# Kernel optimization log

Hardware: AMD Instinct MI355X
Metric: run time of the kernel (lower is better)

## Reference

```python
import jax, jax.numpy as jnp
import numpy as np

WS = 32          # window_size
STRIDE = 16
OUTPUT = 224
GRADE_N = 6

def _dct_mat(size):
    i = np.arange(size)[:, None]
    j = np.arange(size)[None, :]
    scale = np.where(i == 0, np.sqrt(1.0 / size), np.sqrt(2.0 / size))
    return (scale * np.cos((j + 0.5) * np.pi * i / size)).astype(np.float32)

def _gen_filter(start, end, size):
    i = np.arange(size)[:, None]
    j = np.arange(size)[None, :]
    s = i + j
    return np.where((s > end) | (s < start), 0.0, 1.0).astype(np.float32)

# constant (non-learnable) buffers, derived from init hyperparams
_D = jnp.asarray(_dct_mat(WS))                       # [32,32]
_LEVEL_FILT = jnp.asarray(_gen_filter(0, WS * 2, WS))  # level_fliter=[0] -> band (0, 64)
_grade_filts = np.stack([_gen_filter(WS * 2.0 / GRADE_N * i, WS * 2.0 / GRADE_N * (i + 1), WS)
                         for i in range(GRADE_N)])    # [G,32,32]
_ft_num = _grade_filts.sum(axis=(1, 2))               # per-filter normalizer
_weights = (2.0 ** np.arange(GRADE_N)).astype(np.float32)  # w=1, *=2 each pass
_GRADE_FILT_SCALED = jnp.asarray(_grade_filts * (_weights / _ft_num)[:, None, None])  # [G,32,32]

def _unfold(x):
    # x: [B,C,H,W] -> patches [B,L,C,ws,ws], L row-major over (oh, ow), matching torch Unfold
    B, C, H, W = x.shape
    nH = (H - WS) // STRIDE + 1
    nW = (W - WS) // STRIDE + 1
    r = jnp.arange(nH) * STRIDE
    c = jnp.arange(nW) * STRIDE
    rows = r[:, None, None, None] + jnp.arange(WS)[None, None, :, None]  # [nH,1,ws,1]
    cols = c[None, :, None, None] + jnp.arange(WS)[None, None, None, :]  # [1,nW,1,ws]
    p = x[:, :, rows, cols]                       # [B,C,nH,nW,ws,ws]
    p = jnp.transpose(p, (0, 2, 3, 1, 4, 5))      # [B,nH,nW,C,ws,ws]
    return p.reshape(B, nH * nW, C, WS, WS)

def setup_inputs() -> dict:
    key = jax.random.key(0)
    x = jax.random.normal(key, (16, 3, 512, 512), dtype=jnp.float32)
    return {"x": x}

def reference(x):
    B, C, H, W = x.shape
    patches = _unfold(x)                          # [B,L,C,32,32]
    x_dct = _D @ patches @ _D.T                   # batched 32x32 DCT

    # level branch (level_N=1): filter is all-pass band (0,64) but applied faithfully
    level_y = _D.T @ (x_dct * _LEVEL_FILT) @ _D   # [B,L,C,32,32]

    # grading: sum_g w_g/ft_g * sum_{c,i,j} filt_g * log(|dct|+1)
    lx = jnp.log(jnp.abs(x_dct) + 1.0)
    grade = jnp.einsum('blcij,gij->bl', lx, _GRADE_FILT_SCALED)  # [B,L]

    idx = jnp.argsort(grade, axis=-1)             # ascending
    b = jnp.arange(B)
    minmin_i  = idx[:, 0]
    minmin_i1 = idx[:, 1]    # B > 1 branch
    maxmax_i  = idx[:, -1]
    maxmax_i1 = idx[:, -2]   # B > 1 branch

    # gather single patch per image; fold0 with one block == reshape to [B,C,32,32]
    x_minmin  = level_y[b, minmin_i]
    x_maxmax  = level_y[b, maxmax_i]
    x_minmin1 = level_y[b, minmin_i1]
    x_maxmax1 = level_y[b, maxmax_i1]
    return (x_minmin, x_maxmax, x_minmin1, x_maxmax1)
```

## Files before the change

### kernel.cpp

```cpp
#include <hip/hip_runtime.h>
#include <cstdint>

constexpr double kPI = 3.14159265358979323846264338327950288;
constexpr double cos_poly(double x) {
    double x2 = x * x, term = 1.0, sum = 1.0;
    for (int n = 1; n <= 13; ++n) { term *= -x2 / double((2 * n - 1) * (2 * n)); sum += term; }
    return sum;
}
constexpr double cos_idx(int a) {
    a &= 127;
    if (a <= 32)  return  cos_poly(a * kPI / 64.0);
    if (a <= 64)  return -cos_poly((64 - a) * kPI / 64.0);
    if (a <= 96)  return -cos_poly((a - 64) * kPI / 64.0);
    return cos_poly((128 - a) * kPI / 64.0);
}
constexpr double csqrt(double v) {
    double x = 1.0;
    for (int i = 0; i < 60; ++i) x = 0.5 * (x + v / x);
    return x;
}
constexpr float Dij(int i, int j) {
    double sc = (i == 0) ? csqrt(1.0 / 32.0) : 0.25;
    int a = ((2 * j + 1) * i) & 127;
    return (float)(sc * cos_idx(a));
}
struct OddT { float d[256]; };
constexpr OddT make_odd() { OddT t{}; for (int m = 0; m < 16; ++m) for (int k = 0; k < 16; ++k) t.d[m*16+k] = Dij(2*m+1, k); return t; }
struct E8T { float d[64]; };
constexpr E8T make_e0() { E8T t{}; for (int m = 0; m < 8; ++m) for (int k = 0; k < 8; ++k) t.d[m*8+k] = Dij(4*m,   k); return t; }
constexpr E8T make_e2() { E8T t{}; for (int m = 0; m < 8; ++m) for (int k = 0; k < 8; ++k) t.d[m*8+k] = Dij(4*m+2, k); return t; }
struct FTab { float f[64]; };
constexpr FTab make_F() {
    FTab t{};
    const int lo[6] = {0, 11, 22, 32, 43, 54};
    const int hi[6] = {10, 21, 32, 42, 53, 62};
    const int n [6] = {66, 187, 306, 286, 165, 45};
    for (int s = 0; s < 64; ++s) {
        double acc = 0.0, w = 1.0;
        for (int g = 0; g < 6; ++g) { if (s >= lo[g] && s <= hi[g]) acc += w / double(n[g]); w *= 2.0; }
        t.f[s] = (float)acc;
    }
    return t;
}
__device__ constexpr OddT cOdd = make_odd();
__device__ constexpr E8T  cE0  = make_e0();
__device__ constexpr E8T  cE2  = make_e2();
__device__ constexpr FTab cF   = make_F();

#define NP  15376
#define LPB 961

template <typename EMIT>
__device__ __forceinline__ void dct32(const float* __restrict__ v, EMIT&& emit) {
    float e[16], o[16];
    #pragma unroll
    for (int k = 0; k < 16; ++k) { e[k] = v[k] + v[31-k]; o[k] = v[k] - v[31-k]; }
    float ee[8], eo[8];
    #pragma unroll
    for (int k = 0; k < 8; ++k)  { ee[k] = e[k] + e[15-k]; eo[k] = e[k] - e[15-k]; }
    #pragma unroll
    for (int m = 0; m < 16; m += 2) {
        float a = 0.f, b = 0.f;
        #pragma unroll
        for (int k = 0; k < 16; ++k) {
            a = fmaf(cOdd.d[m*16+k],     o[k], a);
            b = fmaf(cOdd.d[(m+1)*16+k], o[k], b);
        }
        emit(2*m+1, a); emit(2*m+3, b);
    }
    #pragma unroll
    for (int m = 0; m < 8; m += 2) {
        float a0 = 0.f, a2 = 0.f, b0 = 0.f, b2 = 0.f;
        #pragma unroll
        for (int k = 0; k < 8; ++k) {
            a0 = fmaf(cE0.d[m*8+k],     ee[k], a0);
            a2 = fmaf(cE2.d[m*8+k],     eo[k], a2);
            b0 = fmaf(cE0.d[(m+1)*8+k], ee[k], b0);
            b2 = fmaf(cE2.d[(m+1)*8+k], eo[k], b2);
        }
        emit(4*m, a0); emit(4*m+2, a2); emit(4*m+4, b0); emit(4*m+6, b2);
    }
}

__global__ __launch_bounds__(64) void k_grade(const float* __restrict__ x,
                                              float* __restrict__ partial) {
    __shared__ float sS[2][32 * 33];
    __shared__ float sF[64];
    const int tid = threadIdx.x, g = tid >> 5, lane = tid & 31;
    sF[tid] = cF.f[tid];

    const int task = blockIdx.x * 2 + g;
    const int b  = task / LPB;
    const int l  = task - b * LPB;
    const int ph = l / 31, pw = l - ph * 31;
    const float* xb = x + (size_t)(b * 3) * 262144 + (ph * 16) * 512 + pw * 16;
    float* S = sS[g];
    float gsum = 0.0f;
    __syncthreads();

    float w[32];
    #pragma unroll
    for (int i = 0; i < 32; ++i) w[i] = sF[lane + i];

    #pragma unroll 1
    for (int c = 0; c < 3; ++c) {
        const float4* row = (const float4*)(xb + c * 262144 + lane * 512);
        float p[32];
        #pragma unroll
        for (int q = 0; q < 8; ++q) {
            float4 f = row[q];
            p[4*q] = f.x; p[4*q+1] = f.y; p[4*q+2] = f.z; p[4*q+3] = f.w;
        }
        dct32(p, [&](int j, float acc) { S[j * 33 + lane] = acc; });
        __syncthreads();

        float u[32];
        #pragma unroll
        for (int j = 0; j < 32; ++j) u[j] = S[lane * 33 + j];
        __syncthreads();
        dct32(u, [&](int i, float z) {
            float lx = __logf(fabsf(z) + 1.0f);
            gsum = fmaf(lx, w[i], gsum);
        });
    }
    #pragma unroll
    for (int off = 16; off > 0; off >>= 1) gsum += __shfl_down(gsum, off, 32);
    if (lane == 0) partial[task] = gsum;
}

__global__ __launch_bounds__(256) void k_selgather(const float* __restrict__ partial,
                                                   const float* __restrict__ x,
                                                   float* __restrict__ out) {
    __shared__ unsigned long long smx1[256], smx2[256], smn1[256], smn2[256];
    __shared__ int ssel[4];
    const int b = blockIdx.x, tid = threadIdx.x;
    unsigned long long mx1 = 0, mx2 = 0, mn1 = ~0ULL, mn2 = ~0ULL;
    for (int l = tid; l < LPB; l += 256) {
        unsigned int bits = __float_as_uint(partial[b * LPB + l]);
        unsigned long long k = ((unsigned long long)bits << 32) | (unsigned int)l;
        if (k > mx1) { mx2 = mx1; mx1 = k; } else if (k > mx2) { mx2 = k; }
        if (k < mn1) { mn2 = mn1; mn1 = k; } else if (k < mn2) { mn2 = k; }
    }
    smx1[tid] = mx1; smx2[tid] = mx2; smn1[tid] = mn1; smn2[tid] = mn2;
    for (int off = 128; off > 0; off >>= 1) {
        __syncthreads();
        if (tid < off) {
            unsigned long long a1 = smx1[tid], a2 = smx2[tid], b1 = smx1[tid + off], b2 = smx2[tid + off];
            unsigned long long lo = a1 < b1 ? a1 : b1, hi = a1 < b1 ? b1 : a1;
            unsigned long long c2 = a2 > b2 ? a2 : b2;
            smx1[tid] = hi; smx2[tid] = lo > c2 ? lo : c2;
            a1 = smn1[tid]; a2 = smn2[tid]; b1 = smn1[tid + off]; b2 = smn2[tid + off];
            lo = a1 < b1 ? a1 : b1; hi = a1 < b1 ? b1 : a1;
            c2 = a2 < b2 ? a2 : b2;
            smn1[tid] = lo; smn2[tid] = hi < c2 ? hi : c2;
        }
    }
    __syncthreads();
    if (tid == 0) {
        ssel[0] = (int)(smn1[0] & 0xffffffffu);
        ssel[1] = (int)(smx1[0] & 0xffffffffu);
        ssel[2] = (int)(smn2[0] & 0xffffffffu);
        ssel[3] = (int)(smx2[0] & 0xffffffffu);
    }
    __syncthreads();

    #pragma unroll
    for (int it = 0; it < 12; ++it) {
        const int q  = it * 256 + tid;
        const int o  = q / 768;
        const int r2 = q - o * 768;
        const int c  = r2 >> 8;
        const int p  = r2 & 255;
        const int i  = p >> 3, j4 = p & 7;
        const int l  = ssel[o];
        const int r0 = (l / 31) * 16, c0 = (l - (l / 31) * 31) * 16;
        const float4 v = *(const float4*)(x + ((size_t)(b * 3 + c) * 512 + r0 + i) * 512 + c0 + 4 * j4);
        *(float4*)(out + (size_t)o * 49152 + b * 3072 + c * 1024 + i * 32 + 4 * j4) = v;
    }
}

extern "C" void kernel_launch(void* const* d_in, const int* in_sizes, int n_in,
                              void* d_out, int out_size, void* d_ws, size_t ws_size,
                              hipStream_t stream) {
    const float* x = (const float*)d_in[0];
    float* out     = (float*)d_out;
    float* partial = (float*)d_ws;
    k_grade    <<<NP / 2, 64,  0, stream>>>(x, partial);
    k_selgather<<<16,     256, 0, stream>>>(partial, x, out);
}
```

Measured before the change: 122.6 us.

## Prefetch next channel, deepen DCT butterfly, vectorize shared reads, fold ln2 into weights

The grading kernel now loads the next channel's row into registers while the current channel's DCT runs, so global-load latency overlaps with compute. The DCT gains a third even/odd butterfly level, which cuts the FMAs needed for the even coefficients. Shared-memory transposed reads use float4 with a stride of 36, and the natural log is replaced by log2 with ln2 folded into the constant weight table. Blocks grow to 128 threads with four patches each, trading more register pressure from the prefetch buffer for fewer instructions and less exposed memory latency.

```diff
diff --git a/kernel.cpp b/kernel.cpp
--- a/kernel.cpp
+++ b/kernel.cpp
@@ -1,7 +1,8 @@
 #include <hip/hip_runtime.h>
 #include <cstdint>
 
-constexpr double kPI = 3.14159265358979323846264338327950288;
+constexpr double kPI  = 3.14159265358979323846264338327950288;
+constexpr double kLN2 = 0.69314718055994530941723212145818;
 constexpr double cos_poly(double x) {
     double x2 = x * x, term = 1.0, sum = 1.0;
     for (int n = 1; n <= 13; ++n) { term *= -x2 / double((2 * n - 1) * (2 * n)); sum += term; }
@@ -27,8 +28,10 @@
 struct OddT { float d[256]; };
 constexpr OddT make_odd() { OddT t{}; for (int m = 0; m < 16; ++m) for (int k = 0; k < 16; ++k) t.d[m*16+k] = Dij(2*m+1, k); return t; }
 struct E8T { float d[64]; };
-constexpr E8T make_e0() { E8T t{}; for (int m = 0; m < 8; ++m) for (int k = 0; k < 8; ++k) t.d[m*8+k] = Dij(4*m,   k); return t; }
 constexpr E8T make_e2() { E8T t{}; for (int m = 0; m < 8; ++m) for (int k = 0; k < 8; ++k) t.d[m*8+k] = Dij(4*m+2, k); return t; }
+struct E4T { float d[16]; };
+constexpr E4T make_ee() { E4T t{}; for (int m = 0; m < 4; ++m) for (int k = 0; k < 4; ++k) t.d[m*4+k] = Dij(8*m,   k); return t; }
+constexpr E4T make_eo() { E4T t{}; for (int m = 0; m < 4; ++m) for (int k = 0; k < 4; ++k) t.d[m*4+k] = Dij(8*m+4, k); return t; }
 struct FTab { float f[64]; };
 constexpr FTab make_F() {
     FTab t{};
@@ -38,17 +41,19 @@
     for (int s = 0; s < 64; ++s) {
         double acc = 0.0, w = 1.0;
         for (int g = 0; g < 6; ++g) { if (s >= lo[g] && s <= hi[g]) acc += w / double(n[g]); w *= 2.0; }
-        t.f[s] = (float)acc;
+        t.f[s] = (float)(acc * kLN2);
     }
     return t;
 }
 __device__ constexpr OddT cOdd = make_odd();
-__device__ constexpr E8T  cE0  = make_e0();
 __device__ constexpr E8T  cE2  = make_e2();
+__device__ constexpr E4T  cEE  = make_ee();
+__device__ constexpr E4T  cEO  = make_eo();
 __device__ constexpr FTab cF   = make_F();
 
 #define NP  15376
 #define LPB 961
+#define SST 36
 
 template <typename EMIT>
 __device__ __forceinline__ void dct32(const float* __restrict__ v, EMIT&& emit) {
@@ -58,6 +63,9 @@
     float ee[8], eo[8];
     #pragma unroll
     for (int k = 0; k < 8; ++k)  { ee[k] = e[k] + e[15-k]; eo[k] = e[k] - e[15-k]; }
+    float eee[4], eeo[4];
+    #pragma unroll
+    for (int k = 0; k < 4; ++k)  { eee[k] = ee[k] + ee[7-k]; eeo[k] = ee[k] - ee[7-k]; }
     #pragma unroll
     for (int m = 0; m < 16; m += 2) {
         float a = 0.f, b = 0.f;
@@ -70,57 +78,81 @@
     }
     #pragma unroll
     for (int m = 0; m < 8; m += 2) {
-        float a0 = 0.f, a2 = 0.f, b0 = 0.f, b2 = 0.f;
+        float a = 0.f, b = 0.f;
         #pragma unroll
         for (int k = 0; k < 8; ++k) {
-            a0 = fmaf(cE0.d[m*8+k],     ee[k], a0);
-            a2 = fmaf(cE2.d[m*8+k],     eo[k], a2);
-            b0 = fmaf(cE0.d[(m+1)*8+k], ee[k], b0);
-            b2 = fmaf(cE2.d[(m+1)*8+k], eo[k], b2);
-        }
-        emit(4*m, a0); emit(4*m+2, a2); emit(4*m+4, b0); emit(4*m+6, b2);
-    }
-}
-
-__global__ __launch_bounds__(64) void k_grade(const float* __restrict__ x,
-                                              float* __restrict__ partial) {
-    __shared__ float sS[2][32 * 33];
+            a = fmaf(cE2.d[m*8+k],     eo[k], a);
+            b = fmaf(cE2.d[(m+1)*8+k], eo[k], b);
+        }
+        emit(4*m+2, a); emit(4*m+6, b);
+    }
+    {
+        float a0=0.f,a1=0.f,a2=0.f,a3=0.f,b0=0.f,b1=0.f,b2=0.f,b3=0.f;
+        #pragma unroll
+        for (int k = 0; k < 4; ++k) {
+            a0 = fmaf(cEE.d[0*4+k], eee[k], a0);
+            a1 = fmaf(cEE.d[1*4+k], eee[k], a1);
+            a2 = fmaf(cEE.d[2*4+k], eee[k], a2);
+            a3 = fmaf(cEE.d[3*4+k], eee[k], a3);
+            b0 = fmaf(cEO.d[0*4+k], eeo[k], b0);
+            b1 = fmaf(cEO.d[1*4+k], eeo[k], b1);
+            b2 = fmaf(cEO.d[2*4+k], eeo[k], b2);
+            b3 = fmaf(cEO.d[3*4+k], eeo[k], b3);
+        }
+        emit(0, a0); emit(8, a1); emit(16, a2); emit(24, a3);
+        emit(4, b0); emit(12, b1); emit(20, b2); emit(28, b3);
+    }
+}
+
+__global__ __launch_bounds__(128) void k_grade(const float* __restrict__ x,
+                                               float* __restrict__ partial) {
+    __shared__ __align__(16) float sS[4][32 * SST];
     __shared__ float sF[64];
     const int tid = threadIdx.x, g = tid >> 5, lane = tid & 31;
-    sF[tid] = cF.f[tid];
-
-    const int task = blockIdx.x * 2 + g;
+    if (tid < 64) sF[tid] = cF.f[tid];
+
+    const int task = blockIdx.x * 4 + g;
     const int b  = task / LPB;
     const int l  = task - b * LPB;
     const int ph = l / 31, pw = l - ph * 31;
-    const float* xb = x + (size_t)(b * 3) * 262144 + (ph * 16) * 512 + pw * 16;
+    const float* cb = x + (size_t)(b * 3) * 262144 + (ph * 16) * 512 + pw * 16 + lane * 512;
     float* S = sS[g];
+    __syncthreads();
+
+    float w[32];
+    #pragma unroll
+    for (int i = 0; i < 32; ++i) w[i] = sF[lane + i];
+
+    float4 cur[8];
+    #pragma unroll
+    for (int q = 0; q < 8; ++q) cur[q] = ((const float4*)cb)[q];
+
     float gsum = 0.0f;
-    __syncthreads();
-
-    float w[32];
-    #pragma unroll
-    for (int i = 0; i < 32; ++i) w[i] = sF[lane + i];
-
     #pragma unroll 1
     for (int c = 0; c < 3; ++c) {
-        const float4* row = (const float4*)(xb + c * 262144 + lane * 512);
         float p[32];
         #pragma unroll
         for (int q = 0; q < 8; ++q) {
-            float4 f = row[q];
+            float4 f = cur[q];
             p[4*q] = f.x; p[4*q+1] = f.y; p[4*q+2] = f.z; p[4*q+3] = f.w;
         }
-        dct32(p, [&](int j, float acc) { S[j * 33 + lane] = acc; });
+        if (c < 2) {
+            cb += 262144;
+            #pragma unroll
+            for (int q = 0; q < 8; ++q) cur[q] = ((const float4*)cb)[q];
+        }
+        dct32(p, [&](int j, float acc) { S[j * SST + lane] = acc; });
         __syncthreads();
 
         float u[32];
         #pragma unroll
-        for (int j = 0; j < 32; ++j) u[j] = S[lane * 33 + j];
+        for (int q = 0; q < 8; ++q) {
+            float4 uu = *(const float4*)&S[lane * SST + 4 * q];
+            u[4*q] = uu.x; u[4*q+1] = uu.y; u[4*q+2] = uu.z; u[4*q+3] = uu.w;
+        }
         __syncthreads();
         dct32(u, [&](int i, float z) {
-            float lx = __logf(fabsf(z) + 1.0f);
-            gsum = fmaf(lx, w[i], gsum);
+            gsum = fmaf(__log2f(fabsf(z) + 1.0f), w[i], gsum);
         });
     }
     #pragma unroll
@@ -185,6 +217,6 @@
     const float* x = (const float*)d_in[0];
     float* out     = (float*)d_out;
     float* partial = (float*)d_ws;
-    k_grade    <<<NP / 2, 64,  0, stream>>>(x, partial);
+    k_grade    <<<NP / 4, 128, 0, stream>>>(x, partial);
     k_selgather<<<16,     256, 0, stream>>>(partial, x, out);
 }
```

Result: faster. 112.0 us (-8.7%).
